# Kernel optimization log

Measured on AMD Instinct MI355X. Metric: run time of the kernel, lower is better.

Reference implementation:

```python
import jax, jax.numpy as jnp
import numpy as np


def setup_inputs() -> dict:
    key = jax.random.key(0)
    k_x, k1, k2, k3 = jax.random.split(key, 4)
    dim, hidden, out_dim = 4096, 8192, 4096
    x = jax.random.normal(k_x, (4, 2048, dim), dtype=jnp.float32)
    # VNNILinear initializes weight = randn(out, in) * 0.02
    w1 = jax.random.normal(k1, (hidden, dim), dtype=jnp.float32) * 0.02
    w2 = jax.random.normal(k2, (out_dim, hidden), dtype=jnp.float32) * 0.02
    w3 = jax.random.normal(k3, (hidden, dim), dtype=jnp.float32) * 0.02
    return {"x": x, "w1": w1, "w2": w2, "w3": w3}


def _quant_linear(x, w):
    """Emulate VNNILinear int8 weight-quantized matmul (inference path).

    Per-output-channel symmetric quant: scale = max|w_row| / 127,
    w_q = round(w / scale) in int8, y = x @ (w_q * scale).T.
    """
    w_max = jnp.clip(jnp.max(jnp.abs(w), axis=1, keepdims=True), 1e-6)  # [out,1]
    scale_w = w_max / 127.0
    w_q = jnp.round(w / scale_w).astype(jnp.int8)
    w_dq = w_q.astype(jnp.float32) * scale_w  # dequantized weight
    return jnp.einsum('bsd,hd->bsh', x, w_dq)


def reference(x, w1, w2, w3):
    # SwiGLU: w2( silu(w1(x)) * w3(x) ), all bias-free, int8 VNNI weight quant
    h = jax.nn.silu(_quant_linear(x, w1)) * _quant_linear(x, w3)  # [B,S,hidden]
    return _quant_linear(h, w2)  # [B,S,out_dim]
```

## Files before the change

### kernel.cpp

```cpp
#include <hip/hip_runtime.h>
#include <hip/hip_bf16.h>
#include <stdint.h>


typedef short bf16x8 __attribute__((ext_vector_type(8)));
typedef float f32x4  __attribute__((ext_vector_type(4)));
typedef float f32x16 __attribute__((ext_vector_type(16)));
typedef int   i32x4  __attribute__((ext_vector_type(4)));
typedef int   i32x16 __attribute__((ext_vector_type(16)));

__device__ __forceinline__ unsigned short f2bf(float f) {
  unsigned u = __builtin_bit_cast(unsigned, f);
  u += 0x7FFFu + ((u >> 16) & 1u);
  return (unsigned short)(u >> 16);
}

#define GLOAD_LDS16(gaddr, laddr)                                             \
  __builtin_amdgcn_global_load_lds(                                           \
      (const __attribute__((address_space(1))) void*)(gaddr),                 \
      (__attribute__((address_space(3))) void*)(laddr), 16, 0, 0)

#define FENCE()      asm volatile("" ::: "memory")
#define BAR()        __builtin_amdgcn_s_barrier()
#define WAIT_LGKM(n) asm volatile("s_waitcnt lgkmcnt(" #n ")" ::: "memory")
#define WAIT_VM8()   asm volatile("s_waitcnt vmcnt(8)" ::: "memory")
#define WAIT_VM4()   asm volatile("s_waitcnt vmcnt(4)" ::: "memory")
#define WAIT_VM3()   asm volatile("s_waitcnt vmcnt(3)" ::: "memory")
#define WAIT_VM0()   asm volatile("s_waitcnt vmcnt(0)" ::: "memory")
#define SFENCE()     __builtin_amdgcn_sched_barrier(0)
#define PRIO1()      __builtin_amdgcn_s_setprio(1)
#define PRIO0()      __builtin_amdgcn_s_setprio(0)


template <int NCH>
__global__ void quant_rows_i8_sp(const float* __restrict__ w,
                                 char* __restrict__ q,
                                 float* __restrict__ scale, float clip) {
  const int cols = NCH * 1024;
  const float* wr = w + (size_t)blockIdx.x * cols;
  char* qr = q + (size_t)blockIdx.x * cols;

  float4 v[NCH];
  float m = 0.f;
#pragma unroll
  for (int j = 0; j < NCH; ++j) {
    v[j] = *reinterpret_cast<const float4*>(wr + threadIdx.x * 4 + j * 1024);
    m = fmaxf(m, fmaxf(fmaxf(fabsf(v[j].x), fabsf(v[j].y)),
                       fmaxf(fabsf(v[j].z), fabsf(v[j].w))));
  }
#pragma unroll
  for (int off = 32; off; off >>= 1) m = fmaxf(m, __shfl_xor(m, off));
  __shared__ float smax[4];
  if ((threadIdx.x & 63) == 0) smax[threadIdx.x >> 6] = m;
  __syncthreads();
  m = fmaxf(fmaxf(smax[0], smax[1]), fmaxf(smax[2], smax[3]));

  const float s = fmaxf(m, clip) / 127.0f;
  if (threadIdx.x == 0) scale[blockIdx.x] = s;
#pragma unroll
  for (int j = 0; j < NCH; ++j) {
    int b0 = (int)rintf(v[j].x / s), b1 = (int)rintf(v[j].y / s);
    int b2 = (int)rintf(v[j].z / s), b3 = (int)rintf(v[j].w / s);
    unsigned pk = (b0 & 0xff) | ((b1 & 0xff) << 8) | ((b2 & 0xff) << 16)
                  | ((b3 & 0xff) << 24);
    *reinterpret_cast<unsigned*>(qr + threadIdx.x * 4 + j * 1024) = pk;
  }
}

template <int NCH>
__global__ void quant_rows_bf16_sp(const float* __restrict__ w,
                                   unsigned short* __restrict__ wq) {
  const int cols = NCH * 1024;
  const float* wr = w + (size_t)blockIdx.x * cols;
  unsigned short* wqr = wq + (size_t)blockIdx.x * cols;

  float4 v[NCH];
  float m = 0.f;
#pragma unroll
  for (int j = 0; j < NCH; ++j) {
    v[j] = *reinterpret_cast<const float4*>(wr + threadIdx.x * 4 + j * 1024);
    m = fmaxf(m, fmaxf(fmaxf(fabsf(v[j].x), fabsf(v[j].y)),
                       fmaxf(fabsf(v[j].z), fabsf(v[j].w))));
  }
#pragma unroll
  for (int off = 32; off; off >>= 1) m = fmaxf(m, __shfl_xor(m, off));
  __shared__ float smax[4];
  if ((threadIdx.x & 63) == 0) smax[threadIdx.x >> 6] = m;
  __syncthreads();
  m = fmaxf(fmaxf(smax[0], smax[1]), fmaxf(smax[2], smax[3]));

  const float s = fmaxf(m, 1e-6f) / 127.0f;
#pragma unroll
  for (int j = 0; j < NCH; ++j) {
    ushort4 o;
    o.x = f2bf(rintf(v[j].x / s) * s);
    o.y = f2bf(rintf(v[j].y / s) * s);
    o.z = f2bf(rintf(v[j].z / s) * s);
    o.w = f2bf(rintf(v[j].w / s) * s);
    *reinterpret_cast<ushort4*>(wqr + threadIdx.x * 4 + j * 1024) = o;
  }
}


__device__ __forceinline__ void xcd_swizzle(int& bx, int& by, int gx, int gy) {
  int nwg = gx * gy;
  int bid = by * gx + bx;
  int cpx = nwg >> 3;
  int s = (bid & 7) * cpx + (bid >> 3);
  by = s / gx;
  bx = s % gx;
}

__global__ __launch_bounds__(512, 4)
void gemm_i8_swiglu_kernel(const char* __restrict__ Aq,
                           const char* __restrict__ B1q,
                           const char* __restrict__ B3q,
                           const float* __restrict__ sx,
                           const float* __restrict__ sw1,
                           const float* __restrict__ sw3,
                           unsigned short* __restrict__ H,
                           int M, int N, int K) {
  __shared__ alignas(1024) char lds[73728];

  int bx = blockIdx.x, by = blockIdx.y;
  xcd_swizzle(bx, by, gridDim.x, gridDim.y);
  const int brow = by * 128, bcol = bx * 128;

  const int t = threadIdx.x, lane = t & 63, w = t >> 6;
  const int wr = w >> 2, wc = w & 3;
  const int l31 = lane & 31, hi = lane >> 5;
  const int NT = K >> 6;

  const int rS = t >> 2;
  const int gcS = ((t & 3) ^ ((t >> 3) & 3)) * 16;
  const char* srcA  = Aq  + (size_t)(brow + rS) * K + gcS;
  const char* srcB1 = B1q + (size_t)(bcol + rS) * K + gcS;
  const char* srcB3 = B3q + (size_t)(bcol + rS) * K + gcS;

#define STAGE_A(soff, kt)                                                     \
  GLOAD_LDS16(srcA + (size_t)(kt) * 64, lds + (soff) + t * 16);
#define STAGE_B(soff, kt)                                                     \
  GLOAD_LDS16(srcB1 + (size_t)(kt) * 64, lds + (soff) + 8192 + t * 16);       \
  GLOAD_LDS16(srcB3 + (size_t)(kt) * 64, lds + (soff) + 16384 + t * 16);

  STAGE_A(0, 0); STAGE_B(0, 0);
  STAGE_A(24576, 1); STAGE_B(24576, 1);
  WAIT_VM3();
  FENCE(); BAR();

  const int sx2 = (l31 >> 1) & 3;
  const int aoff  = (wr * 64 + l31) * 64 + ((hi ^ sx2) * 16);
  const int boff1 = 8192 + (wc * 32 + l31) * 64 + ((hi ^ sx2) * 16);
  const int boff3 = boff1 + 8192;

  i32x16 acc[2][2] = {};
  i32x4 a0[2], b10, b30;
  i32x4 a1[2], b11, b31;

  a0[0] = *reinterpret_cast<const i32x4*>(lds + aoff);
  a0[1] = *reinterpret_cast<const i32x4*>(lds + aoff + 2048);
  b10 = *reinterpret_cast<const i32x4*>(lds + boff1);
  b30 = *reinterpret_cast<const i32x4*>(lds + boff3);

#define MFMA4(ar, b1r, b3r)                                                   \
  acc[0][0] = __builtin_amdgcn_mfma_i32_32x32x32_i8(ar[0], b1r, acc[0][0], 0, 0, 0); \
  acc[0][1] = __builtin_amdgcn_mfma_i32_32x32x32_i8(ar[0], b3r, acc[0][1], 0, 0, 0); \
  acc[1][0] = __builtin_amdgcn_mfma_i32_32x32x32_i8(ar[1], b1r, acc[1][0], 0, 0, 0); \
  acc[1][1] = __builtin_amdgcn_mfma_i32_32x32x32_i8(ar[1], b3r, acc[1][1], 0, 0, 0)

  int sl = 0, sn = 24576, sp = 49152;

  for (int k = 0; k < NT; ++k) {
    const bool pf = (k + 2 < NT);

    a1[0] = *reinterpret_cast<const i32x4*>(lds + sl + (aoff ^ 32));
    a1[1] = *reinterpret_cast<const i32x4*>(lds + sl + (aoff ^ 32) + 2048);
    b11 = *reinterpret_cast<const i32x4*>(lds + sl + (boff1 ^ 32));
    b31 = *reinterpret_cast<const i32x4*>(lds + sl + (boff3 ^ 32));
    if (pf) { STAGE_A(sp, k + 2); }
    WAIT_LGKM(4); SFENCE();
    PRIO1(); MFMA4(a0, b10, b30); PRIO0();

    if (pf) {
      STAGE_B(sp, k + 2);
      WAIT_VM3();
    } else if (k == NT - 2) {
      WAIT_VM0();
    }
    WAIT_LGKM(0);
    FENCE(); BAR();
    if (k + 1 < NT) {
      a0[0] = *reinterpret_cast<const i32x4*>(lds + sn + aoff);
      a0[1] = *reinterpret_cast<const i32x4*>(lds + sn + aoff + 2048);
      b10 = *reinterpret_cast<const i32x4*>(lds + sn + boff1);
      b30 = *reinterpret_cast<const i32x4*>(lds + sn + boff3);
    }
    SFENCE();
    PRIO1(); MFMA4(a1, b11, b31); PRIO0();

    int tmp = sl; sl = sn; sn = sp; sp = tmp;
  }
#undef MFMA4
#undef STAGE_A
#undef STAGE_B

  const int ocol = bcol + wc * 32 + l31;
  const int rowb = brow + wr * 64 + 4 * hi;
  const float sw1c = sw1[ocol], sw3c = sw3[ocol];
#pragma unroll
  for (int m = 0; m < 2; ++m) {
#pragma unroll
    for (int rq = 0; rq < 4; ++rq) {
      const int r0 = rowb + m * 32 + 8 * rq;
      const f32x4 sx4 = *reinterpret_cast<const f32x4*>(sx + r0);
#pragma unroll
      for (int j = 0; j < 4; ++j) {
        float y1 = (float)acc[m][0][rq * 4 + j] * (sx4[j] * sw1c);
        float y3 = (float)acc[m][1][rq * 4 + j] * (sx4[j] * sw3c);
        float hv = (y1 / (1.f + __expf(-y1))) * y3;
        H[(size_t)(r0 + j) * N + ocol] = f2bf(hv);
      }
    }
  }
}

__global__ __launch_bounds__(512, 2)
void gemm_bf16_kernel(const unsigned short* __restrict__ A,
                      const unsigned short* __restrict__ B,
                      float* __restrict__ C, int M, int N, int K) {
  __shared__ alignas(1024) unsigned short lds[65536];

  int bx = blockIdx.x, by = blockIdx.y;
  xcd_swizzle(bx, by, gridDim.x, gridDim.y);
  const int brow = by * 256, bcol = bx * 256;

  const int t = threadIdx.x, lane = t & 63, w = t >> 6;
  const int wr = w >> 2, wc = w & 3;
  const int l31 = lane & 31, hi = lane >> 5;
  const bool wodd = (w & 1);
  const int NT = K >> 5;

  const int rS = t >> 2;
  const int cS = ((t & 3) ^ ((t >> 3) & 3)) * 8;
  const unsigned short* srcA = A + (size_t)(brow + rS) * K + cS;
  const unsigned short* srcB = B + (size_t)(bcol + rS) * K + cS;

#define STAGE_P1(pA_, pB_, sp, ko)                                            \
  if (!wodd) {                                                                \
    GLOAD_LDS16((pA_) + (ko), (sp) + t * 8);                                  \
    GLOAD_LDS16((pA_) + (size_t)128 * K + (ko), (sp) + 4096 + t * 8);         \
  } else {                                                                    \
    GLOAD_LDS16((pB_) + (ko), (sp) + 8192 + t * 8);                           \
    GLOAD_LDS16((pB_) + (size_t)128 * K + (ko), (sp) + 12288 + t * 8);        \
  }
#define STAGE_P2(pA_, pB_, sp, ko)                                            \
  if (wodd) {                                                                 \
    GLOAD_LDS16((pA_) + (ko), (sp) + t * 8);                                  \
    GLOAD_LDS16((pA_) + (size_t)128 * K + (ko), (sp) + 4096 + t * 8);         \
  } else {                                                                    \
    GLOAD_LDS16((pB_) + (ko), (sp) + 8192 + t * 8);                           \
    GLOAD_LDS16((pB_) + (size_t)128 * K + (ko), (sp) + 12288 + t * 8);        \
  }

  STAGE_P1(srcA, srcB, lds, 0);
  STAGE_P2(srcA, srcB, lds, 0);
  STAGE_P1(srcA, srcB, lds + 16384, (size_t)32);
  STAGE_P2(srcA, srcB, lds + 16384, (size_t)32);
  STAGE_P1(srcA, srcB, lds + 32768, (size_t)64);
  STAGE_P2(srcA, srcB, lds + 32768, (size_t)64);
  WAIT_VM8();
  FENCE(); BAR();

  const int sx2 = (l31 >> 1) & 3;
  const int aoff  = (wr * 128 + l31) * 32 + ((hi ^ sx2) * 8);
  const int boff0 = 8192 + (wc * 64 + l31) * 32 + ((hi ^ sx2) * 8);
  const int boff1b = boff0 + 1024;
  const int kx0 = wodd ? 16 : 0;
  const int kx1 = kx0 ^ 16;

  f32x16 acc[4][2] = {};
  bf16x8 a0[4], b00, b01;
  bf16x8 a1[4], b10, b11;

#pragma unroll
  for (int m = 0; m < 4; ++m)
    a0[m] = *reinterpret_cast<const bf16x8*>(&lds[(aoff ^ kx0) + m * 1024]);
  b00 = *reinterpret_cast<const bf16x8*>(&lds[boff0 ^ kx0]);
  b01 = *reinterpret_cast<const bf16x8*>(&lds[boff1b ^ kx0]);

#define MFMA8(ar, bx0, bx1)                                                   \
  acc[0][0] = __builtin_amdgcn_mfma_f32_32x32x16_bf16(ar[0], bx0, acc[0][0], 0, 0, 0); \
  acc[0][1] = __builtin_amdgcn_mfma_f32_32x32x16_bf16(ar[0], bx1, acc[0][1], 0, 0, 0); \
  acc[1][0] = __builtin_amdgcn_mfma_f32_32x32x16_bf16(ar[1], bx0, acc[1][0], 0, 0, 0); \
  acc[1][1] = __builtin_amdgcn_mfma_f32_32x32x16_bf16(ar[1], bx1, acc[1][1], 0, 0, 0); \
  acc[2][0] = __builtin_amdgcn_mfma_f32_32x32x16_bf16(ar[2], bx0, acc[2][0], 0, 0, 0); \
  acc[2][1] = __builtin_amdgcn_mfma_f32_32x32x16_bf16(ar[2], bx1, acc[2][1], 0, 0, 0); \
  acc[3][0] = __builtin_amdgcn_mfma_f32_32x32x16_bf16(ar[3], bx0, acc[3][0], 0, 0, 0); \
  acc[3][1] = __builtin_amdgcn_mfma_f32_32x32x16_bf16(ar[3], bx1, acc[3][1], 0, 0, 0)

  int kb = 0;
  for (; kb < NT - 4; kb += 4) {
    const unsigned short* pA = srcA + (size_t)kb * 32;
    const unsigned short* pB = srcB + (size_t)kb * 32;
#pragma unroll
    for (int s = 0; s < 4; ++s) {
      const unsigned short* sl = lds + s * 16384;
      const unsigned short* sn = lds + (((s + 1) & 3) * 16384);
      unsigned short* sp = lds + (((s + 3) & 3) * 16384);
      const int ko = (s + 3) * 32;

      a1[0] = *reinterpret_cast<const bf16x8*>(sl + (aoff ^ kx1));
      a1[1] = *reinterpret_cast<const bf16x8*>(sl + (aoff ^ kx1) + 1024);
      a1[2] = *reinterpret_cast<const bf16x8*>(sl + (aoff ^ kx1) + 2048);
      a1[3] = *reinterpret_cast<const bf16x8*>(sl + (aoff ^ kx1) + 3072);
      b10 = *reinterpret_cast<const bf16x8*>(sl + (boff0 ^ kx1));
      b11 = *reinterpret_cast<const bf16x8*>(sl + (boff1b ^ kx1));
      STAGE_P1(pA, pB, sp, ko);
      WAIT_LGKM(6); SFENCE();
      PRIO1(); MFMA8(a0, b00, b01); PRIO0();

      STAGE_P2(pA, pB, sp, ko);
      WAIT_VM8();
      WAIT_LGKM(0);
      FENCE(); BAR();
      a0[0] = *reinterpret_cast<const bf16x8*>(sn + (aoff ^ kx0));
      a0[1] = *reinterpret_cast<const bf16x8*>(sn + (aoff ^ kx0) + 1024);
      a0[2] = *reinterpret_cast<const bf16x8*>(sn + (aoff ^ kx0) + 2048);
      a0[3] = *reinterpret_cast<const bf16x8*>(sn + (aoff ^ kx0) + 3072);
      b00 = *reinterpret_cast<const bf16x8*>(sn + (boff0 ^ kx0));
      b01 = *reinterpret_cast<const bf16x8*>(sn + (boff1b ^ kx0));
      SFENCE();
      PRIO1(); MFMA8(a1, b10, b11); PRIO0();
    }
  }

  for (int k = kb; k < NT; ++k) {
    const unsigned short* sl = &lds[(k & 3) * 16384];
    const bool pf = (k + 3 < NT);

    a1[0] = *reinterpret_cast<const bf16x8*>(sl + (aoff ^ kx1));
    a1[1] = *reinterpret_cast<const bf16x8*>(sl + (aoff ^ kx1) + 1024);
    a1[2] = *reinterpret_cast<const bf16x8*>(sl + (aoff ^ kx1) + 2048);
    a1[3] = *reinterpret_cast<const bf16x8*>(sl + (aoff ^ kx1) + 3072);
    b10 = *reinterpret_cast<const bf16x8*>(sl + (boff0 ^ kx1));
    b11 = *reinterpret_cast<const bf16x8*>(sl + (boff1b ^ kx1));
    if (pf) {
      unsigned short* sp = lds + (((k + 3) & 3) * 16384);
      STAGE_P1(srcA, srcB, sp, (size_t)(k + 3) * 32);
    }
    WAIT_LGKM(6); SFENCE();
    PRIO1(); MFMA8(a0, b00, b01); PRIO0();

    if (pf) {
      unsigned short* sp = lds + (((k + 3) & 3) * 16384);
      STAGE_P2(srcA, srcB, sp, (size_t)(k + 3) * 32);
      WAIT_VM8();
    } else if (k == NT - 3) {
      WAIT_VM4();
    } else if (k == NT - 2) {
      WAIT_VM0();
    }
    WAIT_LGKM(0);
    FENCE(); BAR();
    if (k + 1 < NT) {
      const unsigned short* sn = &lds[((k + 1) & 3) * 16384];
      a0[0] = *reinterpret_cast<const bf16x8*>(sn + (aoff ^ kx0));
      a0[1] = *reinterpret_cast<const bf16x8*>(sn + (aoff ^ kx0) + 1024);
      a0[2] = *reinterpret_cast<const bf16x8*>(sn + (aoff ^ kx0) + 2048);
      a0[3] = *reinterpret_cast<const bf16x8*>(sn + (aoff ^ kx0) + 3072);
      b00 = *reinterpret_cast<const bf16x8*>(sn + (boff0 ^ kx0));
      b01 = *reinterpret_cast<const bf16x8*>(sn + (boff1b ^ kx0));
    }
    SFENCE();
    PRIO1(); MFMA8(a1, b10, b11); PRIO0();
  }
#undef MFMA8
#undef STAGE_P1
#undef STAGE_P2

  const int ocol = bcol + wc * 64 + l31;
  const int rowb = brow + wr * 128 + 4 * hi;
#pragma unroll
  for (int m = 0; m < 4; ++m)
#pragma unroll
    for (int n = 0; n < 2; ++n)
#pragma unroll
      for (int rq = 0; rq < 4; ++rq)
#pragma unroll
        for (int j = 0; j < 4; ++j)
          C[(size_t)(rowb + m * 32 + 8 * rq + j) * N + (ocol + n * 32)] =
              acc[m][n][rq * 4 + j];
}


extern "C" void kernel_launch(void* const* d_in, const int* in_sizes, int n_in,
                              void* d_out, int out_size, void* d_ws,
                              size_t ws_size, hipStream_t stream) {
  const float* x  = (const float*)d_in[0];
  const float* w1 = (const float*)d_in[1];
  const float* w2 = (const float*)d_in[2];
  const float* w3 = (const float*)d_in[3];
  float* out = (float*)d_out;

  const int DIM = 4096, HID = 8192;
  const int M = in_sizes[0] / DIM;

  char* xq  = (char*)d_ws;
  char* w1q = xq + (size_t)M * DIM;
  char* w3q = w1q + (size_t)HID * DIM;
  unsigned short* w2b = (unsigned short*)(w3q + (size_t)HID * DIM);
  unsigned short* h = w2b + (size_t)DIM * HID;
  float* sx  = (float*)(h + (size_t)M * HID);
  float* sw1 = sx + M;
  float* sw3 = sw1 + HID;

  quant_rows_i8_sp<4><<<HID, 256, 0, stream>>>(w1, w1q, sw1, 1e-6f);
  quant_rows_i8_sp<4><<<HID, 256, 0, stream>>>(w3, w3q, sw3, 1e-6f);
  quant_rows_i8_sp<4><<<M, 256, 0, stream>>>(x, xq, sx, 1e-30f);
  quant_rows_bf16_sp<8><<<DIM, 256, 0, stream>>>(w2, w2b);

  gemm_i8_swiglu_kernel<<<dim3(HID / 128, M / 128), 512, 0, stream>>>(
      xq, w1q, w3q, sx, sw1, sw3, h, M, HID, DIM);
  gemm_bf16_kernel<<<dim3(DIM / 256, M / 256), 512, 0, stream>>>(
      h, w2b, out, M, DIM, HID);
}
```

Before: 1.314 ms.

## Enlarge int8 SwiGLU tile to 256 rows and load B fragments straight to registers

```diff
diff --git a/kernel.cpp b/kernel.cpp
--- a/kernel.cpp
+++ b/kernel.cpp
@@ -25,7 +25,7 @@
 #define WAIT_LGKM(n) asm volatile("s_waitcnt lgkmcnt(" #n ")" ::: "memory")
 #define WAIT_VM8()   asm volatile("s_waitcnt vmcnt(8)" ::: "memory")
 #define WAIT_VM4()   asm volatile("s_waitcnt vmcnt(4)" ::: "memory")
-#define WAIT_VM3()   asm volatile("s_waitcnt vmcnt(3)" ::: "memory")
+#define WAIT_VM2()   asm volatile("s_waitcnt vmcnt(2)" ::: "memory")
 #define WAIT_VM0()   asm volatile("s_waitcnt vmcnt(0)" ::: "memory")
 #define SFENCE()     __builtin_amdgcn_sched_barrier(0)
 #define PRIO1()      __builtin_amdgcn_s_setprio(1)
@@ -111,7 +111,7 @@
   bx = s % gx;
 }
 
-__global__ __launch_bounds__(512, 4)
+__global__ __launch_bounds__(512, 2)
 void gemm_i8_swiglu_kernel(const char* __restrict__ Aq,
                            const char* __restrict__ B1q,
                            const char* __restrict__ B3q,
@@ -120,11 +120,11 @@
                            const float* __restrict__ sw3,
                            unsigned short* __restrict__ H,
                            int M, int N, int K) {
-  __shared__ alignas(1024) char lds[73728];
+  __shared__ alignas(1024) char lds[49152];
 
   int bx = blockIdx.x, by = blockIdx.y;
   xcd_swizzle(bx, by, gridDim.x, gridDim.y);
-  const int brow = by * 128, bcol = bx * 128;
+  const int brow = by * 256, bcol = bx * 128;
 
   const int t = threadIdx.x, lane = t & 63, w = t >> 6;
   const int wr = w >> 2, wc = w & 3;
@@ -133,82 +133,97 @@
 
   const int rS = t >> 2;
   const int gcS = ((t & 3) ^ ((t >> 3) & 3)) * 16;
-  const char* srcA  = Aq  + (size_t)(brow + rS) * K + gcS;
-  const char* srcB1 = B1q + (size_t)(bcol + rS) * K + gcS;
-  const char* srcB3 = B3q + (size_t)(bcol + rS) * K + gcS;
+  const char* srcA = Aq + (size_t)(brow + rS) * K + gcS;
 
 #define STAGE_A(soff, kt)                                                     \
-  GLOAD_LDS16(srcA + (size_t)(kt) * 64, lds + (soff) + t * 16);
-#define STAGE_B(soff, kt)                                                     \
-  GLOAD_LDS16(srcB1 + (size_t)(kt) * 64, lds + (soff) + 8192 + t * 16);       \
-  GLOAD_LDS16(srcB3 + (size_t)(kt) * 64, lds + (soff) + 16384 + t * 16);
-
-  STAGE_A(0, 0); STAGE_B(0, 0);
-  STAGE_A(24576, 1); STAGE_B(24576, 1);
-  WAIT_VM3();
+  GLOAD_LDS16(srcA + (size_t)(kt) * 64, lds + (soff) + t * 16);               \
+  GLOAD_LDS16(srcA + (size_t)128 * K + (size_t)(kt) * 64,                     \
+              lds + (soff) + 8192 + t * 16);
+
+  const char* gB1f = B1q + (size_t)(bcol + wc * 32 + l31) * K + hi * 16;
+  const char* gB3f = B3q + (size_t)(bcol + wc * 32 + l31) * K + hi * 16;
+
+  const int sx2 = (l31 >> 1) & 3;
+  const int aoff = (wr * 128 + l31) * 64 + ((hi ^ sx2) * 16);
+
+  i32x16 acc[4][2] = {};
+  i32x4 a0[4], a1[4];
+  i32x4 c10, c11, c30, c31;
+  i32x4 n10, n11, n30, n31;
+
+  STAGE_A(0, 0);
+  STAGE_A(16384, 1);
+  STAGE_A(32768, 2);
+  c10 = *reinterpret_cast<const i32x4*>(gB1f);
+  c11 = *reinterpret_cast<const i32x4*>(gB1f + 32);
+  c30 = *reinterpret_cast<const i32x4*>(gB3f);
+  c31 = *reinterpret_cast<const i32x4*>(gB3f + 32);
+  WAIT_VM0();
   FENCE(); BAR();
-
-  const int sx2 = (l31 >> 1) & 3;
-  const int aoff  = (wr * 64 + l31) * 64 + ((hi ^ sx2) * 16);
-  const int boff1 = 8192 + (wc * 32 + l31) * 64 + ((hi ^ sx2) * 16);
-  const int boff3 = boff1 + 8192;
-
-  i32x16 acc[2][2] = {};
-  i32x4 a0[2], b10, b30;
-  i32x4 a1[2], b11, b31;
-
   a0[0] = *reinterpret_cast<const i32x4*>(lds + aoff);
   a0[1] = *reinterpret_cast<const i32x4*>(lds + aoff + 2048);
-  b10 = *reinterpret_cast<const i32x4*>(lds + boff1);
-  b30 = *reinterpret_cast<const i32x4*>(lds + boff3);
-
-#define MFMA4(ar, b1r, b3r)                                                   \
+  a0[2] = *reinterpret_cast<const i32x4*>(lds + aoff + 4096);
+  a0[3] = *reinterpret_cast<const i32x4*>(lds + aoff + 6144);
+
+#define MFMA8(ar, b1r, b3r)                                                   \
   acc[0][0] = __builtin_amdgcn_mfma_i32_32x32x32_i8(ar[0], b1r, acc[0][0], 0, 0, 0); \
   acc[0][1] = __builtin_amdgcn_mfma_i32_32x32x32_i8(ar[0], b3r, acc[0][1], 0, 0, 0); \
   acc[1][0] = __builtin_amdgcn_mfma_i32_32x32x32_i8(ar[1], b1r, acc[1][0], 0, 0, 0); \
-  acc[1][1] = __builtin_amdgcn_mfma_i32_32x32x32_i8(ar[1], b3r, acc[1][1], 0, 0, 0)
-
-  int sl = 0, sn = 24576, sp = 49152;
+  acc[1][1] = __builtin_amdgcn_mfma_i32_32x32x32_i8(ar[1], b3r, acc[1][1], 0, 0, 0); \
+  acc[2][0] = __builtin_amdgcn_mfma_i32_32x32x32_i8(ar[2], b1r, acc[2][0], 0, 0, 0); \
+  acc[2][1] = __builtin_amdgcn_mfma_i32_32x32x32_i8(ar[2], b3r, acc[2][1], 0, 0, 0); \
+  acc[3][0] = __builtin_amdgcn_mfma_i32_32x32x32_i8(ar[3], b1r, acc[3][0], 0, 0, 0); \
+  acc[3][1] = __builtin_amdgcn_mfma_i32_32x32x32_i8(ar[3], b3r, acc[3][1], 0, 0, 0)
+
+  int sl = 0, sn = 16384, sp = 32768;
 
   for (int k = 0; k < NT; ++k) {
-    const bool pf = (k + 2 < NT);
+    const bool pf1 = (k + 1 < NT);
+    const bool pf2 = (k + 2 < NT);
 
     a1[0] = *reinterpret_cast<const i32x4*>(lds + sl + (aoff ^ 32));
     a1[1] = *reinterpret_cast<const i32x4*>(lds + sl + (aoff ^ 32) + 2048);
-    b11 = *reinterpret_cast<const i32x4*>(lds + sl + (boff1 ^ 32));
-    b31 = *reinterpret_cast<const i32x4*>(lds + sl + (boff3 ^ 32));
-    if (pf) { STAGE_A(sp, k + 2); }
+    a1[2] = *reinterpret_cast<const i32x4*>(lds + sl + (aoff ^ 32) + 4096);
+    a1[3] = *reinterpret_cast<const i32x4*>(lds + sl + (aoff ^ 32) + 6144);
+    if (pf1) {
+      const size_t ko = (size_t)(k + 1) * 64;
+      n10 = *reinterpret_cast<const i32x4*>(gB1f + ko);
+      n11 = *reinterpret_cast<const i32x4*>(gB1f + ko + 32);
+      n30 = *reinterpret_cast<const i32x4*>(gB3f + ko);
+      n31 = *reinterpret_cast<const i32x4*>(gB3f + ko + 32);
+    }
+    SFENCE();
+    if (pf2) { STAGE_A(sp, k + 2); }
     WAIT_LGKM(4); SFENCE();
-    PRIO1(); MFMA4(a0, b10, b30); PRIO0();
-
-    if (pf) {
-      STAGE_B(sp, k + 2);
-      WAIT_VM3();
-    } else if (k == NT - 2) {
+    PRIO1(); MFMA8(a0, c10, c30); PRIO0();
+
+    if (pf2) {
+      WAIT_VM2();
+    } else {
       WAIT_VM0();
     }
     WAIT_LGKM(0);
     FENCE(); BAR();
-    if (k + 1 < NT) {
+    if (pf1) {
       a0[0] = *reinterpret_cast<const i32x4*>(lds + sn + aoff);
       a0[1] = *reinterpret_cast<const i32x4*>(lds + sn + aoff + 2048);
-      b10 = *reinterpret_cast<const i32x4*>(lds + sn + boff1);
-      b30 = *reinterpret_cast<const i32x4*>(lds + sn + boff3);
+      a0[2] = *reinterpret_cast<const i32x4*>(lds + sn + aoff + 4096);
+      a0[3] = *reinterpret_cast<const i32x4*>(lds + sn + aoff + 6144);
     }
     SFENCE();
-    PRIO1(); MFMA4(a1, b11, b31); PRIO0();
-
+    PRIO1(); MFMA8(a1, c11, c31); PRIO0();
+
+    c10 = n10; c11 = n11; c30 = n30; c31 = n31;
     int tmp = sl; sl = sn; sn = sp; sp = tmp;
   }
-#undef MFMA4
+#undef MFMA8
 #undef STAGE_A
-#undef STAGE_B
 
   const int ocol = bcol + wc * 32 + l31;
-  const int rowb = brow + wr * 64 + 4 * hi;
+  const int rowb = brow + wr * 128 + 4 * hi;
   const float sw1c = sw1[ocol], sw3c = sw3[ocol];
 #pragma unroll
-  for (int m = 0; m < 2; ++m) {
+  for (int m = 0; m < 4; ++m) {
 #pragma unroll
     for (int rq = 0; rq < 4; ++rq) {
       const int r0 = rowb + m * 32 + 8 * rq;
@@ -419,7 +434,7 @@
   quant_rows_i8_sp<4><<<M, 256, 0, stream>>>(x, xq, sx, 1e-30f);
   quant_rows_bf16_sp<8><<<DIM, 256, 0, stream>>>(w2, w2b);
 
-  gemm_i8_swiglu_kernel<<<dim3(HID / 128, M / 128), 512, 0, stream>>>(
+  gemm_i8_swiglu_kernel<<<dim3(HID / 128, M / 256), 512, 0, stream>>>(
       xq, w1q, w3q, sx, sw1, sw3, h, M, HID, DIM);
   gemm_bf16_kernel<<<dim3(DIM / 256, M / 256), 512, 0, stream>>>(
       h, w2b, out, M, DIM, HID);
```

Result: slower. 1.665 ms (+26.7%).
